# Kernel optimization log

Hardware: AMD Instinct MI355X
Metric: run time of the kernel (lower is better)

## Reference

```python
import jax, jax.numpy as jnp
import numpy as np

N = 50000   # nodes
E = 800000  # directed edges
D = 128     # input_channels


def _kaiming(key, shape):
    fan_in = shape[0]
    return jax.random.normal(key, shape, jnp.float32) * np.float32(np.sqrt(2.0 / fan_in))


def setup_inputs():
    key = jax.random.key(0)
    ks = jax.random.split(key, 8)
    x = jax.random.normal(ks[0], (N, D), jnp.float32)
    edge_index = jax.random.randint(ks[1], (2, E), 0, N, dtype=jnp.int32)
    return {
        "x": x,
        "edge_index": edge_index,
        "W_in": _kaiming(ks[2], (D, D)),      "b_in": jnp.zeros((D,), jnp.float32),
        "W1": _kaiming(ks[3], (D, 2 * D)),    "b1": jnp.zeros((2 * D,), jnp.float32),
        "W2": _kaiming(ks[4], (2 * D, D)),    "b2": jnp.zeros((D,), jnp.float32),
        "W3": _kaiming(ks[5], (D, D // 2)),   "b3": jnp.zeros((D // 2,), jnp.float32),
        "W_out": _kaiming(ks[6], (D // 2, 1)), "b_out": jnp.zeros((1,), jnp.float32),
    }


def _gcn_conv(x, src, dst, W, b, n):
    """PyG GCNConv: add self-loops, symmetric D^-1/2 (A+I) D^-1/2 normalization."""
    h = x @ W  # [n, out]
    loop = jnp.arange(n, dtype=src.dtype)
    s = jnp.concatenate([src, loop])  # message sources (x_j)
    d = jnp.concatenate([dst, loop])  # aggregation targets (x_i)
    deg = jax.ops.segment_sum(jnp.ones_like(d, jnp.float32), d, num_segments=n)
    dis = jnp.where(deg > 0, jax.lax.rsqrt(jnp.maximum(deg, 1.0)), 0.0)
    norm = dis[s] * dis[d]  # [E+n]
    msg = h[s] * norm[:, None]  # gather + scale
    out = jax.ops.segment_sum(msg, d, num_segments=n)  # scatter-add
    return out + b


def reference(x, edge_index, W_in, b_in, W1, b1, W2, b2, W3, b3, W_out, b_out):
    src, dst = edge_index[0], edge_index[1]
    n = x.shape[0]
    lrelu = lambda t: jax.nn.leaky_relu(t, 0.01)
    # dropout in eval mode (identity)
    h = lrelu(x @ W_in + b_in)
    h = lrelu(_gcn_conv(h, src, dst, W1, b1, n))
    h = lrelu(_gcn_conv(h, src, dst, W2, b2, n))
    h = lrelu(_gcn_conv(h, src, dst, W3, b3, n))
    return h @ W_out + b_out  # [n, 1]
```

## Files before the change

### kernel.cpp

```cpp
#include <hip/hip_runtime.h>


#define LRELU(v) ((v) > 0.f ? (v) : 0.01f * (v))

typedef __attribute__((ext_vector_type(8))) _Float16 half8;
typedef __attribute__((ext_vector_type(8))) float float8;
typedef __attribute__((ext_vector_type(4))) float floatx4;

constexpr int CAP = 64;

template <int F>
__device__ __forceinline__ half8 loadB(const float* __restrict__ W, int k0,
                                       int col) {
  half8 h;
#pragma unroll
  for (int j = 0; j < 8; ++j) h[j] = (_Float16)W[(long)(k0 + j) * F + col];
  return h;
}

template <int K, int F, int EPI, typename IT>
__device__ __forceinline__ void gemm_tile(const IT* __restrict__ X,
                                          const float* __restrict__ W,
                                          const float* __restrict__ bias,
                                          const int* __restrict__ cnt,
                                          _Float16* __restrict__ out, int M,
                                          int tile, _Float16* __restrict__ xs) {
  constexpr int TM = 64;
  constexpr int PAD = 8;
  constexpr int LK = K + PAD;
  constexpr int CW = F / 4;
  constexpr int NT = CW / 16;
  constexpr int NK = K / 32;

  const int m0 = tile * TM;
  const int tid = threadIdx.x;
  const int w = tid >> 6;
  const int lane = tid & 63;
  const int m = lane & 15;
  const int q = lane >> 4;

  half8 breg[NT][NK];
#pragma unroll
  for (int t = 0; t < NT; ++t)
#pragma unroll
    for (int kc = 0; kc < NK; ++kc)
      breg[t][kc] = loadB<F>(W, kc * 32 + q * 8, w * CW + t * 16 + m);

  constexpr int CPR = K / 8;
  for (int idx = tid; idx < TM * CPR; idx += 256) {
    const int row = idx / CPR;
    const int kk = idx % CPR;
    const int g = m0 + row;
    half8 h = (half8)(_Float16)0.f;
    if (g < M) {
      if constexpr (sizeof(IT) == 4) {
        const float4* p = (const float4*)&X[(long)g * K + kk * 8];
        float4 a = p[0], cc = p[1];
        h[0] = (_Float16)a.x; h[1] = (_Float16)a.y;
        h[2] = (_Float16)a.z; h[3] = (_Float16)a.w;
        h[4] = (_Float16)cc.x; h[5] = (_Float16)cc.y;
        h[6] = (_Float16)cc.z; h[7] = (_Float16)cc.w;
      } else {
        h = *(const half8*)&X[(long)g * K + kk * 8];
      }
    }
    *(half8*)&xs[row * LK + kk * 8] = h;
  }
  __syncthreads();

  floatx4 acc[4][NT];
#pragma unroll
  for (int rt = 0; rt < 4; ++rt)
#pragma unroll
    for (int t = 0; t < NT; ++t) acc[rt][t] = (floatx4){0.f, 0.f, 0.f, 0.f};

#pragma unroll
  for (int kc = 0; kc < NK; ++kc) {
    half8 af[4];
#pragma unroll
    for (int rt = 0; rt < 4; ++rt)
      af[rt] = *(const half8*)&xs[(rt * 16 + m) * LK + kc * 32 + q * 8];
#pragma unroll
    for (int rt = 0; rt < 4; ++rt)
#pragma unroll
      for (int t = 0; t < NT; ++t)
        acc[rt][t] = __builtin_amdgcn_mfma_f32_16x16x32_f16(af[rt], breg[t][kc],
                                                            acc[rt][t], 0, 0, 0);
  }

#pragma unroll
  for (int rt = 0; rt < 4; ++rt) {
#pragma unroll
    for (int r = 0; r < 4; ++r) {
      const int row = m0 + rt * 16 + q * 4 + r;
      if (row < M) {
        float dv = 1.f;
        if constexpr (EPI == 2) dv = rsqrtf((float)cnt[row] + 1.0f);
#pragma unroll
        for (int t = 0; t < NT; ++t) {
          const int col = w * CW + t * 16 + m;
          float v = acc[rt][t][r];
          if constexpr (EPI == 1) { v += bias[col]; v = LRELU(v); }
          if constexpr (EPI == 2) { v *= dv; }
          out[(long)row * F + col] = (_Float16)v;
        }
      }
    }
  }
}

__global__ __launch_bounds__(256) void k_sg(const float* __restrict__ x,
                                            const float* __restrict__ W_in,
                                            const float* __restrict__ b_in,
                                            const int* __restrict__ src,
                                            const int* __restrict__ dst,
                                            int* __restrict__ cnt,
                                            unsigned short* __restrict__ pad,
                                            _Float16* __restrict__ h0,
                                            int N, int E, int PR,
                                            int gemmBlocks) {
  __shared__ _Float16 xs[64 * 136];
  const int b = blockIdx.x;
  if (b < gemmBlocks) {
    gemm_tile<128, 128, 1, float>(x, W_in, b_in, nullptr, h0, N, b, xs);
  } else {
    const int bb = b - gemmBlocks;
    const int range = bb & 7;
    const int e = (bb >> 3) * 256 + (int)threadIdx.x;
    if (e < E) {
      const int d = dst[e];
      if ((unsigned)(d - range * PR) < (unsigned)PR) {
        const int pos = atomicAdd(&cnt[d], 1);
        if (pos < CAP) pad[(long)d * CAP + pos] = (unsigned short)src[e];
      }
    }
  }
}

__global__ __launch_bounds__(256) void k_gemm3(const _Float16* __restrict__ X,
                                               const float* __restrict__ W3,
                                               const int* __restrict__ cnt,
                                               _Float16* __restrict__ out,
                                               int M) {
  __shared__ _Float16 xs[64 * 136];
  gemm_tile<128, 64, 2, _Float16>(X, W3, nullptr, cnt, out, M, blockIdx.x, xs);
}

__global__ __launch_bounds__(256) void k_g2x(const _Float16* __restrict__ X,
                                             const float* __restrict__ W1,
                                             const float* __restrict__ b1,
                                             const float* __restrict__ W2,
                                             const int* __restrict__ cnt,
                                             _Float16* __restrict__ out, int M) {
  constexpr int LK1 = 128 + 8;
  constexpr int LK2 = 256 + 8;
  __shared__ _Float16 smem[64 * LK2];
  _Float16* xs = smem;
  _Float16* ys = smem;

  const int m0 = blockIdx.x * 64;
  const int tid = threadIdx.x;
  const int w = tid >> 6;
  const int lane = tid & 63;
  const int m = lane & 15;
  const int q = lane >> 4;

  for (int idx = tid; idx < 64 * 16; idx += 256) {
    const int row = idx >> 4;
    const int kk = idx & 15;
    const int g = m0 + row;
    half8 h = (half8)(_Float16)0.f;
    if (g < M) h = *(const half8*)&X[(long)g * 128 + kk * 8];
    *(half8*)&xs[row * LK1 + kk * 8] = h;
  }

  half8 breg1[4][4];
#pragma unroll
  for (int t = 0; t < 4; ++t)
#pragma unroll
    for (int kc = 0; kc < 4; ++kc)
      breg1[t][kc] = loadB<256>(W1, kc * 32 + q * 8, w * 64 + t * 16 + m);

  __syncthreads();

  floatx4 acc1[4][4];
#pragma unroll
  for (int rt = 0; rt < 4; ++rt)
#pragma unroll
    for (int t = 0; t < 4; ++t) acc1[rt][t] = (floatx4){0.f, 0.f, 0.f, 0.f};

#pragma unroll
  for (int kc = 0; kc < 4; ++kc) {
    half8 af[4];
#pragma unroll
    for (int rt = 0; rt < 4; ++rt)
      af[rt] = *(const half8*)&xs[(rt * 16 + m) * LK1 + kc * 32 + q * 8];
#pragma unroll
    for (int rt = 0; rt < 4; ++rt)
#pragma unroll
      for (int t = 0; t < 4; ++t)
        acc1[rt][t] = __builtin_amdgcn_mfma_f32_16x16x32_f16(af[rt], breg1[t][kc],
                                                             acc1[rt][t], 0, 0, 0);
  }

  half8 breg2[2][8];
#pragma unroll
  for (int t = 0; t < 2; ++t)
#pragma unroll
    for (int kc = 0; kc < 8; ++kc)
      breg2[t][kc] = loadB<128>(W2, kc * 32 + q * 8, w * 32 + t * 16 + m);

  __syncthreads();

#pragma unroll
  for (int rt = 0; rt < 4; ++rt) {
#pragma unroll
    for (int r = 0; r < 4; ++r) {
      const int row = rt * 16 + q * 4 + r;
#pragma unroll
      for (int t = 0; t < 4; ++t) {
        const int col = w * 64 + t * 16 + m;
        float v = acc1[rt][t][r] + b1[col];
        ys[row * LK2 + col] = (_Float16)LRELU(v);
      }
    }
  }

  __syncthreads();

  floatx4 acc2[4][2];
#pragma unroll
  for (int rt = 0; rt < 4; ++rt)
#pragma unroll
    for (int t = 0; t < 2; ++t) acc2[rt][t] = (floatx4){0.f, 0.f, 0.f, 0.f};

#pragma unroll
  for (int kc = 0; kc < 8; ++kc) {
    half8 af[4];
#pragma unroll
    for (int rt = 0; rt < 4; ++rt)
      af[rt] = *(const half8*)&ys[(rt * 16 + m) * LK2 + kc * 32 + q * 8];
#pragma unroll
    for (int rt = 0; rt < 4; ++rt)
#pragma unroll
      for (int t = 0; t < 2; ++t)
        acc2[rt][t] = __builtin_amdgcn_mfma_f32_16x16x32_f16(af[rt], breg2[t][kc],
                                                             acc2[rt][t], 0, 0, 0);
  }

#pragma unroll
  for (int rt = 0; rt < 4; ++rt) {
#pragma unroll
    for (int r = 0; r < 4; ++r) {
      const int row = m0 + rt * 16 + q * 4 + r;
      if (row < M) {
        const float dv = rsqrtf((float)cnt[row] + 1.0f);
#pragma unroll
        for (int t = 0; t < 2; ++t) {
          const int col = w * 32 + t * 16 + m;
          out[(long)row * 128 + col] = (_Float16)(acc2[rt][t][r] * dv);
        }
      }
    }
  }
}

__global__ __launch_bounds__(256) void k_agg_pre(const _Float16* __restrict__ G,
                                                 const unsigned short* __restrict__ pad,
                                                 const int* __restrict__ cnt,
                                                 _Float16* __restrict__ out,
                                                 int N) {
  const int w = threadIdx.x >> 6;
  const int lane = threadIdx.x & 63;
  const int c = lane & 15;
  const int jj = lane >> 4;
  int i = blockIdx.x * 4 + w;
  const bool valid = (i < N);
  if (!valid) i = N - 1;
  const int cni = cnt[i];
  const int cn = min(cni, CAP);
  const float dvi = rsqrtf((float)cni + 1.f);
  const _Float16* gb = G + c * 8;
  const unsigned short* pl = pad + (long)i * CAP;

  float8 a0 = {0.f, 0.f, 0.f, 0.f, 0.f, 0.f, 0.f, 0.f};
  float8 a1 = a0, a2 = a0, a3 = a0;
  if (jj == 0) {
    float8 f = __builtin_convertvector(*(const half8*)(gb + (long)i * 128), float8);
#pragma unroll
    for (int k = 0; k < 8; ++k) a0[k] = f[k] * dvi;
  }
  int e = jj;
  for (; e + 12 < cn; e += 16) {
    const int s0 = pl[e], s1 = pl[e + 4], s2 = pl[e + 8], s3 = pl[e + 12];
    const float d0 = rsqrtf((float)cnt[s0] + 1.f);
    const float d1 = rsqrtf((float)cnt[s1] + 1.f);
    const float d2 = rsqrtf((float)cnt[s2] + 1.f);
    const float d3 = rsqrtf((float)cnt[s3] + 1.f);
    float8 f0 = __builtin_convertvector(*(const half8*)(gb + (long)s0 * 128), float8);
    float8 f1 = __builtin_convertvector(*(const half8*)(gb + (long)s1 * 128), float8);
    float8 f2 = __builtin_convertvector(*(const half8*)(gb + (long)s2 * 128), float8);
    float8 f3 = __builtin_convertvector(*(const half8*)(gb + (long)s3 * 128), float8);
#pragma unroll
    for (int k = 0; k < 8; ++k) {
      a0[k] += f0[k] * d0;
      a1[k] += f1[k] * d1;
      a2[k] += f2[k] * d2;
      a3[k] += f3[k] * d3;
    }
  }
  for (; e < cn; e += 4) {
    const int s = pl[e];
    const float d = rsqrtf((float)cnt[s] + 1.f);
    float8 f = __builtin_convertvector(*(const half8*)(gb + (long)s * 128), float8);
#pragma unroll
    for (int k = 0; k < 8; ++k) a0[k] += f[k] * d;
  }
#pragma unroll
  for (int k = 0; k < 8; ++k) a0[k] += a1[k] + a2[k] + a3[k];
#pragma unroll
  for (int k = 0; k < 8; ++k) {
    a0[k] += __shfl_xor(a0[k], 16);
    a0[k] += __shfl_xor(a0[k], 32);
  }
  if (valid && jj == 0) {
    half8 hv;
#pragma unroll
    for (int k = 0; k < 8; ++k) hv[k] = (_Float16)(a0[k] * dvi);
    *(half8*)&out[(long)i * 128 + c * 8] = hv;
  }
}

__global__ __launch_bounds__(256) void k_agg_post(const _Float16* __restrict__ G,
                                                  const unsigned short* __restrict__ pad,
                                                  const int* __restrict__ cnt,
                                                  const float* __restrict__ bias,
                                                  _Float16* __restrict__ out,
                                                  int N) {
  const int w = threadIdx.x >> 6;
  const int lane = threadIdx.x & 63;
  const int c = lane & 15;
  const int jj = lane >> 4;
  int i = blockIdx.x * 4 + w;
  const bool valid = (i < N);
  if (!valid) i = N - 1;
  const int cni = cnt[i];
  const int cn = min(cni, CAP);
  const float dvi = rsqrtf((float)cni + 1.f);
  const _Float16* gb = G + c * 8;
  const unsigned short* pl = pad + (long)i * CAP;

  float8 a0 = {0.f, 0.f, 0.f, 0.f, 0.f, 0.f, 0.f, 0.f};
  float8 a1 = a0, a2 = a0, a3 = a0;
  if (jj == 0)
    a0 = __builtin_convertvector(*(const half8*)(gb + (long)i * 128), float8);
  int e = jj;
  for (; e + 12 < cn; e += 16) {
    const int s0 = pl[e], s1 = pl[e + 4], s2 = pl[e + 8], s3 = pl[e + 12];
    a0 += __builtin_convertvector(*(const half8*)(gb + (long)s0 * 128), float8);
    a1 += __builtin_convertvector(*(const half8*)(gb + (long)s1 * 128), float8);
    a2 += __builtin_convertvector(*(const half8*)(gb + (long)s2 * 128), float8);
    a3 += __builtin_convertvector(*(const half8*)(gb + (long)s3 * 128), float8);
  }
  for (; e < cn; e += 4) {
    const int s = pl[e];
    a0 += __builtin_convertvector(*(const half8*)(gb + (long)s * 128), float8);
  }
  a0 += a1 + a2 + a3;
#pragma unroll
  for (int k = 0; k < 8; ++k) {
    a0[k] += __shfl_xor(a0[k], 16);
    a0[k] += __shfl_xor(a0[k], 32);
  }
  if (valid && jj == 0) {
    half8 hv;
#pragma unroll
    for (int k = 0; k < 8; ++k) {
      float v = a0[k] * dvi + bias[c * 8 + k];
      hv[k] = (_Float16)LRELU(v);
    }
    *(half8*)&out[(long)i * 128 + c * 8] = hv;
  }
}

__global__ __launch_bounds__(256) void k_agg_final(const _Float16* __restrict__ G,
                                                   const unsigned short* __restrict__ pad,
                                                   const int* __restrict__ cnt,
                                                   const float* __restrict__ b3,
                                                   const float* __restrict__ Wout,
                                                   const float* __restrict__ bout,
                                                   float* __restrict__ out, int N) {
  const int w = threadIdx.x >> 6;
  const int lane = threadIdx.x & 63;
  const int c = lane & 7;
  const int j = lane >> 3;
  const int n = j >> 2;
  const int jj = j & 3;
  int i = blockIdx.x * 8 + w * 2 + n;
  const bool valid = (i < N);
  if (!valid) i = N - 1;
  const int cni = cnt[i];
  const int cn = min(cni, CAP);
  const float dvi = rsqrtf((float)cni + 1.f);
  const _Float16* gb = G + c * 8;
  const unsigned short* pl = pad + (long)i * CAP;

  float8 a0 = {0.f, 0.f, 0.f, 0.f, 0.f, 0.f, 0.f, 0.f};
  float8 a1 = a0;
  if (jj == 0)
    a0 = __builtin_convertvector(*(const half8*)(gb + (long)i * 64), float8);
  int e = jj;
  for (; e + 4 < cn; e += 8) {
    const int s0 = pl[e], s1 = pl[e + 4];
    a0 += __builtin_convertvector(*(const half8*)(gb + (long)s0 * 64), float8);
    a1 += __builtin_convertvector(*(const half8*)(gb + (long)s1 * 64), float8);
  }
  if (e < cn)
    a0 += __builtin_convertvector(*(const half8*)(gb + (long)pl[e] * 64), float8);
  a0 += a1;
#pragma unroll
  for (int k = 0; k < 8; ++k) {
    a0[k] += __shfl_xor(a0[k], 8);
    a0[k] += __shfl_xor(a0[k], 16);
  }
  float p = 0.f;
#pragma unroll
  for (int k = 0; k < 8; ++k) {
    const int col = c * 8 + k;
    float v = a0[k] * dvi + b3[col];
    v = LRELU(v);
    p += v * Wout[col];
  }
  p += __shfl_xor(p, 1);
  p += __shfl_xor(p, 2);
  p += __shfl_xor(p, 4);
  if (valid && jj == 0 && c == 0) out[i] = p + bout[0];
}


extern "C" void kernel_launch(void* const* d_in, const int* in_sizes, int n_in,
                              void* d_out, int out_size, void* d_ws, size_t ws_size,
                              hipStream_t stream) {
  const float* x     = (const float*)d_in[0];
  const int* eidx    = (const int*)d_in[1];
  const float* W_in  = (const float*)d_in[2];
  const float* b_in  = (const float*)d_in[3];
  const float* W1    = (const float*)d_in[4];
  const float* b1    = (const float*)d_in[5];
  const float* W2    = (const float*)d_in[6];
  const float* b2    = (const float*)d_in[7];
  const float* W3    = (const float*)d_in[8];
  const float* b3    = (const float*)d_in[9];
  const float* W_out = (const float*)d_in[10];
  const float* b_out = (const float*)d_in[11];
  float* out = (float*)d_out;

  const int N = in_sizes[0] / 128;
  const int E = in_sizes[1] / 2;
  const int* src = eidx;
  const int* dst = eidx + E;
  const int PR = (N + 7) / 8;

  size_t off = 0;
  char* base = (char*)d_ws;
  auto alloc = [&](size_t bytes) -> void* {
    void* p = base + off;
    off = (off + bytes + 255) & ~(size_t)255;
    return p;
  };
  int* cnt            = (int*)alloc((size_t)N * sizeof(int));
  unsigned short* pad = (unsigned short*)alloc((size_t)N * CAP * 2);
  _Float16* buf1      = (_Float16*)alloc((size_t)N * 128 * 2);
  _Float16* buf2      = (_Float16*)alloc((size_t)N * 128 * 2);
  _Float16* buf3      = (_Float16*)alloc((size_t)N * 64 * 2);

  hipMemsetAsync(cnt, 0, (size_t)N * sizeof(int), stream);

  const int gE8 = 8 * ((E + 255) / 256);
  const int gRows = (N + 63) / 64;
  const int gAgg = (N + 3) / 4;
  const int gAggF = (N + 7) / 8;

  k_sg<<<gRows + gE8, 256, 0, stream>>>(x, W_in, b_in, src, dst, cnt, pad,
                                        buf1, N, E, PR, gRows);
  k_agg_pre<<<gAgg, 256, 0, stream>>>(buf1, pad, cnt, buf2, N);
  k_g2x<<<gRows, 256, 0, stream>>>(buf2, W1, b1, W2, cnt, buf1, N);
  k_agg_post<<<gAgg, 256, 0, stream>>>(buf1, pad, cnt, b2, buf2, N);
  k_gemm3<<<gRows, 256, 0, stream>>>(buf2, W3, cnt, buf3, N);
  k_agg_final<<<gAggF, 256, 0, stream>>>(buf3, pad, cnt, b3, W_out, b_out,
                                         out, N);
}
```

Measured before the change: 283.8 us.

## Fuse layer-2 aggregation epilogue with W3 matmul and reorder scatter/GEMM blocks

Merges the post-aggregation kernel with the third GEMM: each wave computes the activated 128-wide row in registers and multiplies it by W3 with fp32 FMAs and shuffle reductions, writing the pre-scaled 64-wide output directly. This removes one launch and the fp16 round trip of the intermediate N×128 buffer. It costs scalar FMA work and many shuffles instead of matrix-core MFMA. The scatter phase also moves to a fixed 2048-block grid-stride loop placed ahead of the GEMM blocks.

```diff
diff --git a/kernel.cpp b/kernel.cpp
--- a/kernel.cpp
+++ b/kernel.cpp
@@ -117,33 +117,28 @@
                                             int* __restrict__ cnt,
                                             unsigned short* __restrict__ pad,
                                             _Float16* __restrict__ h0,
-                                            int N, int E, int PR,
-                                            int gemmBlocks) {
+                                            int N, int E, int PR, int nScat) {
   __shared__ _Float16 xs[64 * 136];
   const int b = blockIdx.x;
-  if (b < gemmBlocks) {
-    gemm_tile<128, 128, 1, float>(x, W_in, b_in, nullptr, h0, N, b, xs);
-  } else {
-    const int bb = b - gemmBlocks;
-    const int range = bb & 7;
-    const int e = (bb >> 3) * 256 + (int)threadIdx.x;
-    if (e < E) {
-      const int d = dst[e];
-      if ((unsigned)(d - range * PR) < (unsigned)PR) {
-        const int pos = atomicAdd(&cnt[d], 1);
-        if (pos < CAP) pad[(long)d * CAP + pos] = (unsigned short)src[e];
+  if (b < nScat) {
+    const int range = b & 7;
+    const int lo = range * PR;
+    const int gE = (E + 255) >> 8;
+    const int step = nScat >> 3;
+    const int tid = threadIdx.x;
+    for (int ch = b >> 3; ch < gE; ch += step) {
+      const int e = ch * 256 + tid;
+      if (e < E) {
+        const int d = dst[e];
+        if ((unsigned)(d - lo) < (unsigned)PR) {
+          const int pos = atomicAdd(&cnt[d], 1);
+          if (pos < CAP) pad[(long)d * CAP + pos] = (unsigned short)src[e];
+        }
       }
     }
-  }
-}
-
-__global__ __launch_bounds__(256) void k_gemm3(const _Float16* __restrict__ X,
-                                               const float* __restrict__ W3,
-                                               const int* __restrict__ cnt,
-                                               _Float16* __restrict__ out,
-                                               int M) {
-  __shared__ _Float16 xs[64 * 136];
-  gemm_tile<128, 64, 2, _Float16>(X, W3, nullptr, cnt, out, M, blockIdx.x, xs);
+  } else {
+    gemm_tile<128, 128, 1, float>(x, W_in, b_in, nullptr, h0, N, b - nScat, xs);
+  }
 }
 
 __global__ __launch_bounds__(256) void k_g2x(const _Float16* __restrict__ X,
@@ -331,12 +326,13 @@
   }
 }
 
-__global__ __launch_bounds__(256) void k_agg_post(const _Float16* __restrict__ G,
-                                                  const unsigned short* __restrict__ pad,
-                                                  const int* __restrict__ cnt,
-                                                  const float* __restrict__ bias,
-                                                  _Float16* __restrict__ out,
-                                                  int N) {
+__global__ __launch_bounds__(256) void k_aggmm(const _Float16* __restrict__ G,
+                                               const unsigned short* __restrict__ pad,
+                                               const int* __restrict__ cnt,
+                                               const float* __restrict__ b2,
+                                               const float* __restrict__ W3,
+                                               _Float16* __restrict__ out,
+                                               int N) {
   const int w = threadIdx.x >> 6;
   const int lane = threadIdx.x & 63;
   const int c = lane & 15;
@@ -372,15 +368,38 @@
     a0[k] += __shfl_xor(a0[k], 16);
     a0[k] += __shfl_xor(a0[k], 32);
   }
-  if (valid && jj == 0) {
-    half8 hv;
-#pragma unroll
-    for (int k = 0; k < 8; ++k) {
-      float v = a0[k] * dvi + bias[c * 8 + k];
-      hv[k] = (_Float16)LRELU(v);
-    }
-    *(half8*)&out[(long)i * 128 + c * 8] = hv;
-  }
+
+  float h2v[8];
+#pragma unroll
+  for (int k = 0; k < 8; ++k) {
+    float v = a0[k] * dvi + b2[c * 8 + k];
+    h2v[k] = LRELU(v);
+  }
+
+  float p[16];
+#pragma unroll
+  for (int t = 0; t < 16; ++t) p[t] = 0.f;
+#pragma unroll
+  for (int j = 0; j < 8; ++j) {
+    const float4* wr = (const float4*)&W3[(long)(c * 8 + j) * 64 + jj * 16];
+    const float hv = h2v[j];
+    float4 w0 = wr[0], w1 = wr[1], w2 = wr[2], w3v = wr[3];
+    p[0] += hv * w0.x;  p[1] += hv * w0.y;  p[2] += hv * w0.z;  p[3] += hv * w0.w;
+    p[4] += hv * w1.x;  p[5] += hv * w1.y;  p[6] += hv * w1.z;  p[7] += hv * w1.w;
+    p[8] += hv * w2.x;  p[9] += hv * w2.y;  p[10] += hv * w2.z; p[11] += hv * w2.w;
+    p[12] += hv * w3v.x; p[13] += hv * w3v.y; p[14] += hv * w3v.z; p[15] += hv * w3v.w;
+  }
+#pragma unroll
+  for (int k = 0; k < 4; ++k) {
+    const int bit = 1 << k;
+#pragma unroll
+    for (int t = 0; t < 16; ++t) p[t] += __shfl_xor(p[t], bit);
+  }
+  float r = p[0];
+#pragma unroll
+  for (int t = 1; t < 16; ++t)
+    if (c == t) r = p[t];
+  if (valid) out[(long)i * 64 + jj * 16 + c] = (_Float16)(dvi * r);
 }
 
 __global__ __launch_bounds__(256) void k_agg_final(const _Float16* __restrict__ G,
@@ -476,17 +495,16 @@
 
   hipMemsetAsync(cnt, 0, (size_t)N * sizeof(int), stream);
 
-  const int gE8 = 8 * ((E + 255) / 256);
+  const int nScat = 2048;
   const int gRows = (N + 63) / 64;
   const int gAgg = (N + 3) / 4;
   const int gAggF = (N + 7) / 8;
 
-  k_sg<<<gRows + gE8, 256, 0, stream>>>(x, W_in, b_in, src, dst, cnt, pad,
-                                        buf1, N, E, PR, gRows);
+  k_sg<<<nScat + gRows, 256, 0, stream>>>(x, W_in, b_in, src, dst, cnt, pad,
+                                          buf1, N, E, PR, nScat);
   k_agg_pre<<<gAgg, 256, 0, stream>>>(buf1, pad, cnt, buf2, N);
   k_g2x<<<gRows, 256, 0, stream>>>(buf2, W1, b1, W2, cnt, buf1, N);
-  k_agg_post<<<gAgg, 256, 0, stream>>>(buf1, pad, cnt, b2, buf2, N);
-  k_gemm3<<<gRows, 256, 0, stream>>>(buf2, W3, cnt, buf3, N);
+  k_aggmm<<<gAgg, 256, 0, stream>>>(buf1, pad, cnt, b2, W3, buf3, N);
   k_agg_final<<<gAggF, 256, 0, stream>>>(buf3, pad, cnt, b3, W_out, b_out,
                                          out, N);
 }
```

Result: slower. 420.8 us (+48.2%).

## Interleave edge bucketing with GEMM tiles and split aggregation by column halves

Applied to the files above, without the earlier changes.

The fused scatter/GEMM kernel now uses a fixed grid of groups. Half the blocks in each group loop over edge chunks with vectorized int4 loads of src/dst for one destination range, and the other half run input-GEMM tiles, interleaved. The pre/post aggregation kernels split the feature columns into two 64-wide halves, each processed by separate blocks that handle 8 nodes each with narrower shuffles. This aims to balance the GEMM and atomic-bucketing work and raise parallelism in the gather kernels. The cost is that each column half re-reads the neighbour lists and degree counts.

```diff
diff --git a/kernel.cpp b/kernel.cpp
--- a/kernel.cpp
+++ b/kernel.cpp
@@ -117,23 +117,56 @@
                                             int* __restrict__ cnt,
                                             unsigned short* __restrict__ pad,
                                             _Float16* __restrict__ h0,
-                                            int N, int E, int PR,
-                                            int gemmBlocks) {
+                                            int N, int E, int PR, int nGroups,
+                                            int gemmTiles) {
   __shared__ _Float16 xs[64 * 136];
   const int b = blockIdx.x;
-  if (b < gemmBlocks) {
-    gemm_tile<128, 128, 1, float>(x, W_in, b_in, nullptr, h0, N, b, xs);
+  const int g = b >> 4;
+  const int r = b & 15;
+  if (r < 8) {
+    const int lo = r * PR;
+    const int tid = threadIdx.x;
+    if ((E & 3) == 0) {
+      const int nCh = E >> 10;
+      for (int ch = g; ch < nCh; ch += nGroups) {
+        const int e0 = ch * 1024 + tid * 4;
+        const int4 d4 = *(const int4*)&dst[e0];
+        const int4 s4 = *(const int4*)&src[e0];
+#pragma unroll
+        for (int k = 0; k < 4; ++k) {
+          const int d = (&d4.x)[k];
+          if ((unsigned)(d - lo) < (unsigned)PR) {
+            const int pos = atomicAdd(&cnt[d], 1);
+            if (pos < CAP) pad[(long)d * CAP + pos] = (unsigned short)(&s4.x)[k];
+          }
+        }
+      }
+      if (g == 0) {
+        for (int e = (nCh << 10) + tid; e < E; e += 256) {
+          const int d = dst[e];
+          if ((unsigned)(d - lo) < (unsigned)PR) {
+            const int pos = atomicAdd(&cnt[d], 1);
+            if (pos < CAP) pad[(long)d * CAP + pos] = (unsigned short)src[e];
+          }
+        }
+      }
+    } else {
+      const int nCh = (E + 255) >> 8;
+      for (int ch = g; ch < nCh; ch += nGroups) {
+        const int e = ch * 256 + tid;
+        if (e < E) {
+          const int d = dst[e];
+          if ((unsigned)(d - lo) < (unsigned)PR) {
+            const int pos = atomicAdd(&cnt[d], 1);
+            if (pos < CAP) pad[(long)d * CAP + pos] = (unsigned short)src[e];
+          }
+        }
+      }
+    }
   } else {
-    const int bb = b - gemmBlocks;
-    const int range = bb & 7;
-    const int e = (bb >> 3) * 256 + (int)threadIdx.x;
-    if (e < E) {
-      const int d = dst[e];
-      if ((unsigned)(d - range * PR) < (unsigned)PR) {
-        const int pos = atomicAdd(&cnt[d], 1);
-        if (pos < CAP) pad[(long)d * CAP + pos] = (unsigned short)src[e];
-      }
-    }
+    const int tile = g * 8 + (r - 8);
+    if (tile < gemmTiles)
+      gemm_tile<128, 128, 1, float>(x, W_in, b_in, nullptr, h0, N, tile, xs);
   }
 }
 
@@ -269,18 +302,25 @@
                                                  const unsigned short* __restrict__ pad,
                                                  const int* __restrict__ cnt,
                                                  _Float16* __restrict__ out,
-                                                 int N) {
+                                                 int N, int gHalf) {
+  const int b = blockIdx.x;
+  const int ph = (b >= gHalf) ? 1 : 0;
+  const int blk = b - ph * gHalf;
+  const int col0 = ph << 6;
+
   const int w = threadIdx.x >> 6;
   const int lane = threadIdx.x & 63;
-  const int c = lane & 15;
-  const int jj = lane >> 4;
-  int i = blockIdx.x * 4 + w;
+  const int c = lane & 7;
+  const int j = lane >> 3;
+  const int n = j >> 2;
+  const int jj = j & 3;
+  int i = blk * 8 + w * 2 + n;
   const bool valid = (i < N);
   if (!valid) i = N - 1;
   const int cni = cnt[i];
   const int cn = min(cni, CAP);
   const float dvi = rsqrtf((float)cni + 1.f);
-  const _Float16* gb = G + c * 8;
+  const _Float16* gb = G + col0 + c * 8;
   const unsigned short* pl = pad + (long)i * CAP;
 
   float8 a0 = {0.f, 0.f, 0.f, 0.f, 0.f, 0.f, 0.f, 0.f};
@@ -320,14 +360,14 @@
   for (int k = 0; k < 8; ++k) a0[k] += a1[k] + a2[k] + a3[k];
 #pragma unroll
   for (int k = 0; k < 8; ++k) {
+    a0[k] += __shfl_xor(a0[k], 8);
     a0[k] += __shfl_xor(a0[k], 16);
-    a0[k] += __shfl_xor(a0[k], 32);
   }
   if (valid && jj == 0) {
     half8 hv;
 #pragma unroll
     for (int k = 0; k < 8; ++k) hv[k] = (_Float16)(a0[k] * dvi);
-    *(half8*)&out[(long)i * 128 + c * 8] = hv;
+    *(half8*)&out[(long)i * 128 + col0 + c * 8] = hv;
   }
 }
 
@@ -336,18 +376,25 @@
                                                   const int* __restrict__ cnt,
                                                   const float* __restrict__ bias,
                                                   _Float16* __restrict__ out,
-                                                  int N) {
+                                                  int N, int gHalf) {
+  const int b = blockIdx.x;
+  const int ph = (b >= gHalf) ? 1 : 0;
+  const int blk = b - ph * gHalf;
+  const int col0 = ph << 6;
+
   const int w = threadIdx.x >> 6;
   const int lane = threadIdx.x & 63;
-  const int c = lane & 15;
-  const int jj = lane >> 4;
-  int i = blockIdx.x * 4 + w;
+  const int c = lane & 7;
+  const int j = lane >> 3;
+  const int n = j >> 2;
+  const int jj = j & 3;
+  int i = blk * 8 + w * 2 + n;
   const bool valid = (i < N);
   if (!valid) i = N - 1;
   const int cni = cnt[i];
   const int cn = min(cni, CAP);
   const float dvi = rsqrtf((float)cni + 1.f);
-  const _Float16* gb = G + c * 8;
+  const _Float16* gb = G + col0 + c * 8;
   const unsigned short* pl = pad + (long)i * CAP;
 
   float8 a0 = {0.f, 0.f, 0.f, 0.f, 0.f, 0.f, 0.f, 0.f};
@@ -369,17 +416,17 @@
   a0 += a1 + a2 + a3;
 #pragma unroll
   for (int k = 0; k < 8; ++k) {
+    a0[k] += __shfl_xor(a0[k], 8);
     a0[k] += __shfl_xor(a0[k], 16);
-    a0[k] += __shfl_xor(a0[k], 32);
   }
   if (valid && jj == 0) {
     half8 hv;
 #pragma unroll
     for (int k = 0; k < 8; ++k) {
-      float v = a0[k] * dvi + bias[c * 8 + k];
+      float v = a0[k] * dvi + bias[col0 + c * 8 + k];
       hv[k] = (_Float16)LRELU(v);
     }
-    *(half8*)&out[(long)i * 128 + c * 8] = hv;
+    *(half8*)&out[(long)i * 128 + col0 + c * 8] = hv;
   }
 }
 
@@ -476,16 +523,16 @@
 
   hipMemsetAsync(cnt, 0, (size_t)N * sizeof(int), stream);
 
-  const int gE8 = 8 * ((E + 255) / 256);
+  const int nGroups = 256;
   const int gRows = (N + 63) / 64;
-  const int gAgg = (N + 3) / 4;
+  const int gHalf = (N + 7) / 8;
   const int gAggF = (N + 7) / 8;
 
-  k_sg<<<gRows + gE8, 256, 0, stream>>>(x, W_in, b_in, src, dst, cnt, pad,
-                                        buf1, N, E, PR, gRows);
-  k_agg_pre<<<gAgg, 256, 0, stream>>>(buf1, pad, cnt, buf2, N);
+  k_sg<<<nGroups * 16, 256, 0, stream>>>(x, W_in, b_in, src, dst, cnt, pad,
+                                         buf1, N, E, PR, nGroups, gRows);
+  k_agg_pre<<<2 * gHalf, 256, 0, stream>>>(buf1, pad, cnt, buf2, N, gHalf);
   k_g2x<<<gRows, 256, 0, stream>>>(buf2, W1, b1, W2, cnt, buf1, N);
-  k_agg_post<<<gAgg, 256, 0, stream>>>(buf1, pad, cnt, b2, buf2, N);
+  k_agg_post<<<2 * gHalf, 256, 0, stream>>>(buf1, pad, cnt, b2, buf2, N, gHalf);
   k_gemm3<<<gRows, 256, 0, stream>>>(buf2, W3, cnt, buf3, N);
   k_agg_final<<<gAggF, 256, 0, stream>>>(buf3, pad, cnt, b3, W_out, b_out,
                                          out, N);
```

Result: no change. 286.4 us (+0.9%).
